# Kernel tuning notes

Hardware: AMD Instinct MI355X
Metric: run time of the kernel (lower is better)

Reference implementation:

```python
import jax
import jax.numpy as jnp
from jax import lax
import numpy as np

IN_CH, HID, GROUPS = 1024, 256, 8
B, H, W = 16, 64, 64
CPG = HID // GROUPS  # channels per group = 32
EPS = 1e-5


def setup_inputs() -> dict:
    key = jax.random.key(0)
    ks = jax.random.split(key, 8)
    s = 0.02  # small init scale so activations stay well-behaved
    return {
        "x": jax.random.normal(ks[0], (B, IN_CH, H, W), jnp.float32),
        "ctx_w": jax.random.normal(ks[1], (HID, IN_CH), jnp.float32) * s,
        "ctx_b": jnp.zeros((HID,), jnp.float32),
        "kg_w1": jax.random.normal(ks[2], (2 * HID, HID), jnp.float32) * s,
        "kg_b1": jnp.zeros((2 * HID,), jnp.float32),
        "kg_w2": jax.random.normal(ks[3], (GROUPS * 9, 2 * HID), jnp.float32) * s,
        "kg_b2": jnp.zeros((GROUPS * 9,), jnp.float32),
        "in_w": jax.random.normal(ks[4], (HID, IN_CH), jnp.float32) * s,
        "in_b": jnp.zeros((HID,), jnp.float32),
        "out_w": jax.random.normal(ks[5], (HID, HID), jnp.float32) * s,
        "out_b": jnp.zeros((HID,), jnp.float32),
        "gamma": jnp.ones((HID,), jnp.float32),
        "beta": jnp.zeros((HID,), jnp.float32),
    }


def reference(x, ctx_w, ctx_b, kg_w1, kg_b1, kg_w2, kg_b2,
              in_w, in_b, out_w, out_b, gamma, beta):
    b = x.shape[0]
    # context pooling: global avg pool -> 1x1 conv -> relu
    ctx = jnp.mean(x, axis=(2, 3))                       # [B, C_in]
    ctx = jax.nn.relu(ctx @ ctx_w.T + ctx_b)             # [B, HID]
    # kernel generator MLP -> per-sample per-group 3x3 kernels
    hddn = jax.nn.relu(ctx @ kg_w1.T + kg_b1)            # [B, 2*HID]
    kernels = (hddn @ kg_w2.T + kg_b2).reshape(b, GROUPS, 3, 3)
    # input transform (1x1 conv)
    xt = jnp.einsum('bchw,oc->bohw', x, in_w) + in_b[None, :, None, None]
    # expand group kernels to per-channel depthwise kernels [B, HID, 3, 3]
    kch = jnp.repeat(kernels, CPG, axis=1)
    # per-sample depthwise 3x3 conv, padding=1
    def dwconv(xi, ki):  # xi: [HID, H, W], ki: [HID, 3, 3]
        return lax.conv_general_dilated(
            xi[None], ki[:, None], window_strides=(1, 1), padding='SAME',
            dimension_numbers=('NCHW', 'OIHW', 'NCHW'),
            feature_group_count=HID)[0]
    out = jax.vmap(dwconv)(xt, kch)                      # [B, HID, H, W]
    # output transform (1x1 conv)
    out = jnp.einsum('bchw,oc->bohw', out, out_w) + out_b[None, :, None, None]
    # BatchNorm2d (training-mode batch statistics)
    mean = jnp.mean(out, axis=(0, 2, 3))
    var = jnp.var(out, axis=(0, 2, 3))
    out = gamma[None, :, None, None] * (out - mean[None, :, None, None]) \
          * lax.rsqrt(var[None, :, None, None] + EPS) + beta[None, :, None, None]
    return xt + out
```

## Files before the change

### kernel.cpp

```cpp
#include <hip/hip_runtime.h>

#define BATCH 16
#define CIN   1024
#define HID   256
#define HW    4096

typedef __attribute__((ext_vector_type(8))) short bf16x8;
typedef __attribute__((ext_vector_type(4))) float f32x4;

struct __align__(16) f4  { float v[4]; };
struct __align__(8)  us4 { unsigned short v[4]; };
struct __align__(16) us8 { unsigned short v[8]; };

__device__ __forceinline__ float bf2f(unsigned short u) {
  unsigned int x = ((unsigned int)u) << 16;
  return __builtin_bit_cast(float, x);
}
__device__ __forceinline__ unsigned short f2bf(float f) {
  unsigned int u = __builtin_bit_cast(unsigned int, f);
  u += 0x7fff + ((u >> 16) & 1);
  return (unsigned short)(u >> 16);
}

#define LGWB() do { __builtin_amdgcn_sched_barrier(0); \
  asm volatile("s_waitcnt lgkmcnt(0)" ::: "memory"); \
  __builtin_amdgcn_s_barrier(); \
  __builtin_amdgcn_sched_barrier(0); } while (0)

__global__ __launch_bounds__(256)
void prep_kernel(const float* __restrict__ A1, unsigned short* __restrict__ O1,
                 const float* __restrict__ A2, unsigned short* __restrict__ O2,
                 float* __restrict__ zbuf)
{
  const int bidx = blockIdx.x;
  if (bidx >= 160) {
    int idx = (bidx - 160) * 256 + threadIdx.x;
    if (idx < 16896) zbuf[idx] = 0.f;
    return;
  }
  const float* A; unsigned short* O; int KD, u;
  if (bidx < 128) { A = A1; O = O1; KD = 1024; u = bidx * 256 + threadIdx.x; }
  else            { A = A2; O = O2; KD = 256;  u = (bidx - 128) * 256 + threadIdx.x; }
  const int t    = u >> 11;
  const int r    = u & 2047;
  const int wm   = r >> 9, kk = (r >> 8) & 1, mi = (r >> 6) & 3, lane = r & 63;
  const int row  = wm * 64 + mi * 16 + (lane & 15);
  const int k    = t * 64 + kk * 32 + (lane >> 4) * 8;
  f4 v0 = *(const f4*)(A + (size_t)row * KD + k);
  f4 v1 = *(const f4*)(A + (size_t)row * KD + k + 4);
  us8 w = { f2bf(v0.v[0]), f2bf(v0.v[1]), f2bf(v0.v[2]), f2bf(v0.v[3]),
            f2bf(v1.v[0]), f2bf(v1.v[1]), f2bf(v1.v[2]), f2bf(v1.v[3]) };
  *(us8*)(O + (size_t)u * 8) = w;
}

__global__ __launch_bounds__(512, 2)
void gemm1_kernel(const unsigned short* __restrict__ Afrag, const float* __restrict__ xb,
                  const float* __restrict__ bias, unsigned short* __restrict__ Cout,
                  float* __restrict__ ctx_sum)
{
  constexpr int NT = 16;
  __shared__ unsigned short B_sh[2][128 * 64];
  __shared__ float ctx_lds[1024];

  const int tid  = threadIdx.x;
  const int lane = tid & 63;
  const int wv   = tid >> 6;
  const int wm   = wv >> 1, wn = wv & 1;
  const int lr   = lane & 15, lg = lane >> 4;
  const int hi   = lane >> 5, q = lane & 31;

  const int b    = blockIdx.x >> 5;
  const int pix0 = (blockIdx.x & 31) << 7;

  for (int i = tid; i < 1024; i += 512) ctx_lds[i] = 0.f;
  __syncthreads();

  f32x4 acc[4][4] = {};
  const size_t rowbase = ((size_t)b * CIN + 8 * wv + hi) * HW + pix0 + 4 * q;
  const char*  abase   = (const char*)Afrag + wm * 8192 + lane * 16;

  bf16x8 aA[8], aB[8];
  f4 rfA[4], rfB[4];

  auto ISSUE_A = [&](int t, bf16x8* a) {
    const char* p = abase + t * 32768;
    #pragma unroll
    for (int i = 0; i < 8; ++i) a[i] = *(const bf16x8*)(p + i * 1024);
  };
  auto LOADB = [&](int t, f4* rf) {
    const float* p = xb + rowbase + (size_t)t * 64 * HW;
    #pragma unroll
    for (int i = 0; i < 4; ++i) rf[i] = *(const f4*)(p + (size_t)(2 * i) * HW);
  };
  auto WRITEB = [&](int sel, int t, f4* rf) {
    #pragma unroll
    for (int i = 0; i < 4; ++i) {
      float s = rf[i].v[0] + rf[i].v[1] + rf[i].v[2] + rf[i].v[3];
      #pragma unroll
      for (int m = 1; m < 32; m <<= 1) s += __shfl_xor(s, m, 64);
      if (q == 0) atomicAdd(&ctx_lds[t * 64 + 8 * wv + 2 * i + hi], s);
    }
    unsigned int u[4][2];
    #pragma unroll
    for (int i = 0; i < 4; ++i) {
      asm("v_cvt_pk_bf16_f32 %0, %1, %2" : "=v"(u[i][0]) : "v"(rf[i].v[0]), "v"(rf[i].v[1]));
      asm("v_cvt_pk_bf16_f32 %0, %1, %2" : "=v"(u[i][1]) : "v"(rf[i].v[2]), "v"(rf[i].v[3]));
    }
    unsigned int w[4][2];
    #pragma unroll
    for (int i = 0; i < 4; ++i) {
      w[i][0] = __shfl_xor(u[i][0], 32, 64);
      w[i][1] = __shfl_xor(u[i][1], 32, 64);
    }
    #pragma unroll
    for (int jj = 0; jj < 2; ++jj) {
      unsigned int A0 = hi ? w[2][jj] : u[0][jj];
      unsigned int A1 = hi ? u[2][jj] : w[0][jj];
      unsigned int A2 = hi ? w[3][jj] : u[1][jj];
      unsigned int A3 = hi ? u[3][jj] : w[1][jj];
      #pragma unroll
      for (int sub = 0; sub < 2; ++sub) {
        unsigned int lo, h2;
        if (sub == 0) { lo = (A0 & 0xffffu) | (A1 << 16);  h2 = (A2 & 0xffffu) | (A3 << 16); }
        else          { lo = (A0 >> 16) | (A1 & 0xffff0000u); h2 = (A2 >> 16) | (A3 & 0xffff0000u); }
        int p  = 4 * q + jj * 2 + sub;
        int fx = ((p >> 2) ^ p) & 7;
        int byte = p * 128 + (((wv ^ fx) & 7) << 4) + hi * 8;
        uint2 val; val.x = lo; val.y = h2;
        *(uint2*)((char*)B_sh[sel] + byte) = val;
      }
    }
  };
  auto COMPUTE = [&](int sel, bf16x8* a) {
    #pragma unroll
    for (int kk = 0; kk < 2; ++kk) {
      bf16x8 bfr[4];
      #pragma unroll
      for (int ni = 0; ni < 4; ++ni) {
        int pr = wn * 64 + ni * 16 + lr;
        int fx = ((pr >> 2) ^ pr) & 7;
        int byte = pr * 128 + ((((kk * 4 + lg) ^ fx) & 7) << 4);
        bfr[ni] = *(const bf16x8*)((const char*)B_sh[sel] + byte);
      }
      #pragma unroll
      for (int mi = 0; mi < 4; ++mi)
        #pragma unroll
        for (int ni = 0; ni < 4; ++ni)
          acc[mi][ni] = __builtin_amdgcn_mfma_f32_16x16x32_bf16(a[kk * 4 + mi], bfr[ni], acc[mi][ni], 0, 0, 0);
    }
  };

  ISSUE_A(0, aA);
  LOADB(0, rfA);
  LOADB(1, rfB);

  #pragma unroll
  for (int t = 0; t < NT; t += 2) {
    WRITEB(0, t, rfA);
    ISSUE_A(t + 1, aB);
    __builtin_amdgcn_sched_barrier(0);
    if (t + 2 < NT) LOADB(t + 2, rfA);
    LGWB();
    COMPUTE(0, aA);
    WRITEB(1, t + 1, rfB);
    if (t + 2 < NT) ISSUE_A(t + 2, aA);
    __builtin_amdgcn_sched_barrier(0);
    if (t + 3 < NT) LOADB(t + 3, rfB);
    LGWB();
    COMPUTE(1, aB);
  }

  #pragma unroll
  for (int mi = 0; mi < 4; ++mi) {
    #pragma unroll
    for (int r = 0; r < 4; ++r) {
      int o = wm * 64 + mi * 16 + lg * 4 + r;
      float bo = bias[o];
      #pragma unroll
      for (int ni = 0; ni < 4; ++ni) {
        int pix = pix0 + wn * 64 + ni * 16 + lr;
        Cout[((size_t)(b * HID + o)) * HW + pix] = f2bf(acc[mi][ni][r] + bo);
      }
    }
  }
  __syncthreads();
  for (int e = tid; e < 1024; e += 512)
    atomicAdd(&ctx_sum[(size_t)b * 1024 + e], ctx_lds[e]);
}

__global__ __launch_bounds__(512, 2)
void gemm2_fused_kernel(const unsigned short* __restrict__ Afrag,
                        const unsigned short* __restrict__ xt,
                        const float* __restrict__ kern, const float* __restrict__ bias,
                        unsigned short* __restrict__ Cout, float* __restrict__ bn_sums)
{
  constexpr int NT = 4;
  __shared__ unsigned short B_sh[128 * 64];
  __shared__ unsigned short xs[64 * 260];
  __shared__ float kf_s[72];
  __shared__ float bn_lds[512];

  const int tid  = threadIdx.x;
  const int lane = tid & 63;
  const int wv   = tid >> 6;
  const int wm   = wv >> 1, wn = wv & 1;
  const int lr   = lane & 15, lg = lane >> 4;

  const int b    = blockIdx.x >> 5;
  const int R    = blockIdx.x & 31;
  const int pix0 = R << 7;
  const int g0   = R << 1;

  if (tid < 512) bn_lds[tid] = 0.f;
  if (tid < 72)  kf_s[tid] = kern[b * 72 + tid];
  __syncthreads();

  f32x4 acc[4][4] = {};
  const int c4 = tid & 15, q = tid >> 4;
  const int prow  = q >> 4;
  const int pcol4 = (q & 15) << 2;
  const int grp9  = (c4 >> 3) * 9;

  const char* abase = (const char*)Afrag + wm * 8192 + lane * 16;

  bf16x8 aA[8];
  us8 rx[4];

  auto PREXS = [&](int t) {
    #pragma unroll
    for (int it = 0; it < 4; ++it) {
      int flat = it * 512 + tid;
      int ch = flat >> 5, r4 = (flat >> 3) & 3, c8 = flat & 7;
      int grow = g0 - 1 + r4;
      if ((unsigned)grow < 64u) {
        rx[it] = *(const us8*)(xt + ((size_t)(b * HID + t * 64 + ch) << 12) + grow * 64 + c8 * 8);
      } else {
        us8 z = {0, 0, 0, 0, 0, 0, 0, 0}; rx[it] = z;
      }
    }
  };
  auto WRXS = [&]() {
    #pragma unroll
    for (int it = 0; it < 4; ++it) {
      int flat = it * 512 + tid;
      int ch = flat >> 5, r4 = (flat >> 3) & 3, c8 = flat & 7;
      int o = ch * 260 + r4 * 64 + c8 * 8;
      *(us4*)(xs + o)     = *(const us4*)(&rx[it].v[0]);
      *(us4*)(xs + o + 4) = *(const us4*)(&rx[it].v[4]);
    }
  };
  auto ISSUE_A = [&](int t) {
    const char* p = abase + t * 32768;
    #pragma unroll
    for (int i = 0; i < 8; ++i) aA[i] = *(const bf16x8*)(p + i * 1024);
  };

  PREXS(0);
  ISSUE_A(0);

  for (int t = 0; t < NT; ++t) {
    WRXS();
    LGWB();
    if (t + 1 < NT) PREXS(t + 1);
    {
      const float k0 = kf_s[2 * t * 9 + grp9 + 0], k1 = kf_s[2 * t * 9 + grp9 + 1], k2 = kf_s[2 * t * 9 + grp9 + 2];
      const float k3 = kf_s[2 * t * 9 + grp9 + 3], k4 = kf_s[2 * t * 9 + grp9 + 4], k5 = kf_s[2 * t * 9 + grp9 + 5];
      const float k6 = kf_s[2 * t * 9 + grp9 + 6], k7 = kf_s[2 * t * 9 + grp9 + 7], k8 = kf_s[2 * t * 9 + grp9 + 8];
      float dwv[4][4];
      #pragma unroll
      for (int i = 0; i < 4; ++i) {
        int ch = 4 * c4 + i;
        #pragma unroll
        for (int j = 0; j < 4; ++j) dwv[i][j] = 0.f;
        #pragma unroll
        for (int ky = 0; ky < 3; ++ky) {
          int ro = ch * 260 + (prow + ky) * 64;
          float v[6];
          unsigned int p0 = (pcol4 > 0)  ? *(const unsigned int*)(xs + ro + pcol4 - 2) : 0u;
          unsigned int p1 = *(const unsigned int*)(xs + ro + pcol4);
          unsigned int p2 = *(const unsigned int*)(xs + ro + pcol4 + 2);
          unsigned int p3 = (pcol4 < 60) ? *(const unsigned int*)(xs + ro + pcol4 + 4) : 0u;
          v[0] = bf2f((unsigned short)(p0 >> 16));
          v[1] = bf2f((unsigned short)(p1 & 0xffff));
          v[2] = bf2f((unsigned short)(p1 >> 16));
          v[3] = bf2f((unsigned short)(p2 & 0xffff));
          v[4] = bf2f((unsigned short)(p2 >> 16));
          v[5] = bf2f((unsigned short)(p3 & 0xffff));
          float ka = (ky == 0) ? k0 : (ky == 1) ? k3 : k6;
          float kb = (ky == 0) ? k1 : (ky == 1) ? k4 : k7;
          float kc = (ky == 0) ? k2 : (ky == 1) ? k5 : k8;
          #pragma unroll
          for (int j = 0; j < 4; ++j)
            dwv[i][j] += v[j] * ka + v[j + 1] * kb + v[j + 2] * kc;
        }
      }
      #pragma unroll
      for (int j = 0; j < 4; ++j) {
        int pix = 4 * q + j;
        us4 w = { f2bf(dwv[0][j]), f2bf(dwv[1][j]), f2bf(dwv[2][j]), f2bf(dwv[3][j]) };
        *(us4*)((char*)B_sh + pix * 128 + ((8 * c4) ^ ((pix & 7) << 4))) = w;
      }
    }
    LGWB();
    #pragma unroll
    for (int kk = 0; kk < 2; ++kk) {
      bf16x8 bfr[4];
      #pragma unroll
      for (int ni = 0; ni < 4; ++ni) {
        int pr = wn * 64 + ni * 16 + lr;
        bfr[ni] = *(const bf16x8*)((const char*)B_sh + pr * 128 + ((((kk << 2) | lg) ^ (pr & 7)) << 4));
      }
      #pragma unroll
      for (int mi = 0; mi < 4; ++mi)
        #pragma unroll
        for (int ni = 0; ni < 4; ++ni)
          acc[mi][ni] = __builtin_amdgcn_mfma_f32_16x16x32_bf16(aA[kk * 4 + mi], bfr[ni], acc[mi][ni], 0, 0, 0);
    }
    if (t + 1 < NT) ISSUE_A(t + 1);
  }

  #pragma unroll
  for (int mi = 0; mi < 4; ++mi) {
    #pragma unroll
    for (int r = 0; r < 4; ++r) {
      int o = wm * 64 + mi * 16 + lg * 4 + r;
      float bo = bias[o];
      float s = 0.f, s2 = 0.f;
      #pragma unroll
      for (int ni = 0; ni < 4; ++ni) {
        int pix = pix0 + wn * 64 + ni * 16 + lr;
        float val = acc[mi][ni][r] + bo;
        Cout[((size_t)(b * HID + o)) * HW + pix] = f2bf(val);
        s += val; s2 += val * val;
      }
      #pragma unroll
      for (int msk = 1; msk < 16; msk <<= 1) {
        s  += __shfl_xor(s,  msk, 64);
        s2 += __shfl_xor(s2, msk, 64);
      }
      if (lr == 0) { atomicAdd(&bn_lds[o], s); atomicAdd(&bn_lds[256 + o], s2); }
    }
  }
  __syncthreads();
  if (tid < 512) atomicAdd(&bn_sums[tid], bn_lds[tid]);
}

template<int K, int N, bool RELU>
__global__ __launch_bounds__(256)
void fc_kernel(const float* __restrict__ in, const float* __restrict__ w,
               const float* __restrict__ bias, float* __restrict__ out, float scale)
{
  const int wid  = (blockIdx.x << 2) | (threadIdx.x >> 6);
  const int lane = threadIdx.x & 63;
  const int b = wid / N, o = wid - b * N;
  const float* ip = in + (size_t)b * K;
  const float* wp = w  + (size_t)o * K;
  float p = 0.f;
  #pragma unroll
  for (int k = 0; k < K / 64; ++k) p += ip[lane + k * 64] * wp[lane + k * 64];
  #pragma unroll
  for (int m = 1; m < 64; m <<= 1) p += __shfl_xor(p, m, 64);
  if (lane == 0) {
    float v = p * scale + bias[o];
    out[(size_t)b * N + o] = RELU ? fmaxf(v, 0.f) : v;
  }
}

__global__ __launch_bounds__(256)
void final_kernel(const unsigned short* __restrict__ xt, const unsigned short* __restrict__ ot,
                  const float* __restrict__ bn_sums, const float* __restrict__ gamma,
                  const float* __restrict__ beta, float* __restrict__ out)
{
  __shared__ float sc_s[256], sh_s[256];
  {
    int t = threadIdx.x;
    const float inv_n = 1.f / 65536.f;
    float m  = bn_sums[t] * inv_n;
    float v  = bn_sums[256 + t] * inv_n - m * m;
    float sc = gamma[t] * rsqrtf(v + 1e-5f);
    sc_s[t] = sc;
    sh_s[t] = beta[t] - m * sc;
  }
  __syncthreads();
  int g8 = blockIdx.x * 256 + threadIdx.x;
  const int stride8 = 4096 * 256;
  #pragma unroll
  for (int it = 0; it < 2; ++it, g8 += stride8) {
    int o = (g8 >> 9) & 255;
    us8 a = ((const us8*)xt)[g8];
    us8 c = ((const us8*)ot)[g8];
    float s = sc_s[o], h = sh_s[o];
    f4 r0, r1;
    #pragma unroll
    for (int j = 0; j < 4; ++j) r0.v[j] = bf2f(a.v[j])     + s * bf2f(c.v[j])     + h;
    #pragma unroll
    for (int j = 0; j < 4; ++j) r1.v[j] = bf2f(a.v[4 + j]) + s * bf2f(c.v[4 + j]) + h;
    *(f4*)(out + (size_t)g8 * 8)     = r0;
    *(f4*)(out + (size_t)g8 * 8 + 4) = r1;
  }
}

extern "C" void kernel_launch(void* const* d_in, const int* in_sizes, int n_in,
                              void* d_out, int out_size, void* d_ws, size_t ws_size,
                              hipStream_t stream)
{
  const float* x     = (const float*)d_in[0];
  const float* ctx_w = (const float*)d_in[1];
  const float* ctx_b = (const float*)d_in[2];
  const float* kg_w1 = (const float*)d_in[3];
  const float* kg_b1 = (const float*)d_in[4];
  const float* kg_w2 = (const float*)d_in[5];
  const float* kg_b2 = (const float*)d_in[6];
  const float* in_w  = (const float*)d_in[7];
  const float* in_b  = (const float*)d_in[8];
  const float* out_w = (const float*)d_in[9];
  const float* out_b = (const float*)d_in[10];
  const float* gamma = (const float*)d_in[11];
  const float* beta  = (const float*)d_in[12];
  float* out = (float*)d_out;

  char* ws = (char*)d_ws;
  unsigned short* xt = (unsigned short*)ws;
  unsigned short* ot = (unsigned short*)(ws + 33554432);
  float* ctx_sum = (float*)(ws + 67108864);
  float* bn_sums = ctx_sum + 16384;
  float* kern    = bn_sums + 512;
  float* ctxbuf  = kern + 1152;
  float* hddnbuf = ctxbuf + 4096;
  unsigned short* afrag1 = (unsigned short*)(ws + 67108864 + 131072);
  unsigned short* afrag2 = (unsigned short*)(ws + 67108864 + 131072 + 524288);

  prep_kernel<<<226, 256, 0, stream>>>(in_w, afrag1, out_w, afrag2, ctx_sum);
  gemm1_kernel<<<512, 512, 0, stream>>>(afrag1, x, in_b, xt, ctx_sum);
  fc_kernel<1024, 256, true ><<<1024, 256, 0, stream>>>(ctx_sum, ctx_w, ctx_b, ctxbuf, 1.f / 4096.f);
  fc_kernel< 256, 512, true ><<<2048, 256, 0, stream>>>(ctxbuf,  kg_w1, kg_b1, hddnbuf, 1.f);
  fc_kernel< 512,  72, false><<< 288, 256, 0, stream>>>(hddnbuf, kg_w2, kg_b2, kern,    1.f);
  gemm2_fused_kernel<<<512, 512, 0, stream>>>(afrag2, xt, kern, out_b, ot, bn_sums);
  final_kernel<<<4096, 256, 0, stream>>>(xt, ot, bn_sums, gamma, beta, out);
}
```

Baseline: 162.2 us.

## Shrink gemm1 tile to 64 pixels with 4 waves and simpler B staging

```diff
diff --git a/kernel.cpp b/kernel.cpp
--- a/kernel.cpp
+++ b/kernel.cpp
@@ -53,31 +53,31 @@
   *(us8*)(O + (size_t)u * 8) = w;
 }
 
-__global__ __launch_bounds__(512, 2)
+__global__ __launch_bounds__(256, 4)
 void gemm1_kernel(const unsigned short* __restrict__ Afrag, const float* __restrict__ xb,
                   const float* __restrict__ bias, unsigned short* __restrict__ Cout,
                   float* __restrict__ ctx_sum)
 {
   constexpr int NT = 16;
-  __shared__ unsigned short B_sh[2][128 * 64];
+  __shared__ unsigned short B_sh[2][64 * 64];
   __shared__ float ctx_lds[1024];
 
   const int tid  = threadIdx.x;
   const int lane = tid & 63;
   const int wv   = tid >> 6;
-  const int wm   = wv >> 1, wn = wv & 1;
   const int lr   = lane & 15, lg = lane >> 4;
-  const int hi   = lane >> 5, q = lane & 31;
-
-  const int b    = blockIdx.x >> 5;
-  const int pix0 = (blockIdx.x & 31) << 7;
-
-  for (int i = tid; i < 1024; i += 512) ctx_lds[i] = 0.f;
+  const int g    = lane >> 4;
+  const int pq   = lane & 15;
+
+  const int b    = blockIdx.x >> 6;
+  const int pix0 = (blockIdx.x & 63) << 6;
+
+  for (int i = tid; i < 1024; i += 256) ctx_lds[i] = 0.f;
   __syncthreads();
 
   f32x4 acc[4][4] = {};
-  const size_t rowbase = ((size_t)b * CIN + 8 * wv + hi) * HW + pix0 + 4 * q;
-  const char*  abase   = (const char*)Afrag + wm * 8192 + lane * 16;
+  const size_t rowbase = ((size_t)b * CIN + 16 * wv + 4 * g) * HW + pix0 + 4 * pq;
+  const char*  abase   = (const char*)Afrag + wv * 8192 + lane * 16;
 
   bf16x8 aA[8], aB[8];
   f4 rfA[4], rfB[4];
@@ -90,45 +90,30 @@
   auto LOADB = [&](int t, f4* rf) {
     const float* p = xb + rowbase + (size_t)t * 64 * HW;
     #pragma unroll
-    for (int i = 0; i < 4; ++i) rf[i] = *(const f4*)(p + (size_t)(2 * i) * HW);
+    for (int i = 0; i < 4; ++i) rf[i] = *(const f4*)(p + (size_t)i * HW);
   };
   auto WRITEB = [&](int sel, int t, f4* rf) {
     #pragma unroll
     for (int i = 0; i < 4; ++i) {
       float s = rf[i].v[0] + rf[i].v[1] + rf[i].v[2] + rf[i].v[3];
-      #pragma unroll
-      for (int m = 1; m < 32; m <<= 1) s += __shfl_xor(s, m, 64);
-      if (q == 0) atomicAdd(&ctx_lds[t * 64 + 8 * wv + 2 * i + hi], s);
-    }
-    unsigned int u[4][2];
-    #pragma unroll
-    for (int i = 0; i < 4; ++i) {
-      asm("v_cvt_pk_bf16_f32 %0, %1, %2" : "=v"(u[i][0]) : "v"(rf[i].v[0]), "v"(rf[i].v[1]));
-      asm("v_cvt_pk_bf16_f32 %0, %1, %2" : "=v"(u[i][1]) : "v"(rf[i].v[2]), "v"(rf[i].v[3]));
-    }
-    unsigned int w[4][2];
-    #pragma unroll
-    for (int i = 0; i < 4; ++i) {
-      w[i][0] = __shfl_xor(u[i][0], 32, 64);
-      w[i][1] = __shfl_xor(u[i][1], 32, 64);
-    }
-    #pragma unroll
-    for (int jj = 0; jj < 2; ++jj) {
-      unsigned int A0 = hi ? w[2][jj] : u[0][jj];
-      unsigned int A1 = hi ? u[2][jj] : w[0][jj];
-      unsigned int A2 = hi ? w[3][jj] : u[1][jj];
-      unsigned int A3 = hi ? u[3][jj] : w[1][jj];
-      #pragma unroll
-      for (int sub = 0; sub < 2; ++sub) {
-        unsigned int lo, h2;
-        if (sub == 0) { lo = (A0 & 0xffffu) | (A1 << 16);  h2 = (A2 & 0xffffu) | (A3 << 16); }
-        else          { lo = (A0 >> 16) | (A1 & 0xffff0000u); h2 = (A2 >> 16) | (A3 & 0xffff0000u); }
-        int p  = 4 * q + jj * 2 + sub;
-        int fx = ((p >> 2) ^ p) & 7;
-        int byte = p * 128 + (((wv ^ fx) & 7) << 4) + hi * 8;
-        uint2 val; val.x = lo; val.y = h2;
-        *(uint2*)((char*)B_sh[sel] + byte) = val;
-      }
+      s += __shfl_xor(s, 1, 64);
+      s += __shfl_xor(s, 2, 64);
+      s += __shfl_xor(s, 4, 64);
+      s += __shfl_xor(s, 8, 64);
+      if (pq == 0) atomicAdd(&ctx_lds[t * 64 + 16 * wv + 4 * g + i], s);
+    }
+    const int kq = 4 * wv + g;
+    const int slot = kq >> 1, half = kq & 1;
+    #pragma unroll
+    for (int j = 0; j < 4; ++j) {
+      unsigned int lo, hi2;
+      asm("v_cvt_pk_bf16_f32 %0, %1, %2" : "=v"(lo)  : "v"(rf[0].v[j]), "v"(rf[1].v[j]));
+      asm("v_cvt_pk_bf16_f32 %0, %1, %2" : "=v"(hi2) : "v"(rf[2].v[j]), "v"(rf[3].v[j]));
+      int px = 4 * pq + j;
+      int fx = ((px >> 2) ^ px) & 7;
+      int byte = px * 128 + (((slot ^ fx) & 7) << 4) + half * 8;
+      uint2 val; val.x = lo; val.y = hi2;
+      *(uint2*)((char*)B_sh[sel] + byte) = val;
     }
   };
   auto COMPUTE = [&](int sel, bf16x8* a) {
@@ -137,7 +122,7 @@
       bf16x8 bfr[4];
       #pragma unroll
       for (int ni = 0; ni < 4; ++ni) {
-        int pr = wn * 64 + ni * 16 + lr;
+        int pr = ni * 16 + lr;
         int fx = ((pr >> 2) ^ pr) & 7;
         int byte = pr * 128 + ((((kk * 4 + lg) ^ fx) & 7) << 4);
         bfr[ni] = *(const bf16x8*)((const char*)B_sh[sel] + byte);
@@ -174,17 +159,17 @@
   for (int mi = 0; mi < 4; ++mi) {
     #pragma unroll
     for (int r = 0; r < 4; ++r) {
-      int o = wm * 64 + mi * 16 + lg * 4 + r;
+      int o = wv * 64 + mi * 16 + lg * 4 + r;
       float bo = bias[o];
       #pragma unroll
       for (int ni = 0; ni < 4; ++ni) {
-        int pix = pix0 + wn * 64 + ni * 16 + lr;
+        int pix = pix0 + ni * 16 + lr;
         Cout[((size_t)(b * HID + o)) * HW + pix] = f2bf(acc[mi][ni][r] + bo);
       }
     }
   }
   __syncthreads();
-  for (int e = tid; e < 1024; e += 512)
+  for (int e = tid; e < 1024; e += 256)
     atomicAdd(&ctx_sum[(size_t)b * 1024 + e], ctx_lds[e]);
 }
 
@@ -431,7 +416,7 @@
   unsigned short* afrag2 = (unsigned short*)(ws + 67108864 + 131072 + 524288);
 
   prep_kernel<<<226, 256, 0, stream>>>(in_w, afrag1, out_w, afrag2, ctx_sum);
-  gemm1_kernel<<<512, 512, 0, stream>>>(afrag1, x, in_b, xt, ctx_sum);
+  gemm1_kernel<<<1024, 256, 0, stream>>>(afrag1, x, in_b, xt, ctx_sum);
   fc_kernel<1024, 256, true ><<<1024, 256, 0, stream>>>(ctx_sum, ctx_w, ctx_b, ctxbuf, 1.f / 4096.f);
   fc_kernel< 256, 512, true ><<<2048, 256, 0, stream>>>(ctxbuf,  kg_w1, kg_b1, hddnbuf, 1.f);
   fc_kernel< 512,  72, false><<< 288, 256, 0, stream>>>(hddnbuf, kg_w2, kg_b2, kern,    1.f);
```

New measurement: 545.2 us. 236% more time.
